# Performance work log

Hardware: AMD Instinct MI355X
Metric: run time of the kernel (lower is better)

Reference implementation:

```python
import jax, jax.numpy as jnp
import numpy as np

RES = 64

TRI_TABLE = jnp.array([
    [-1,-1,-1,-1,-1,-1],[1,0,2,-1,-1,-1],[4,0,3,-1,-1,-1],[1,4,2,1,3,4],
    [3,1,5,-1,-1,-1],[2,3,0,2,5,3],[1,4,0,1,5,4],[4,2,5,-1,-1,-1],
    [4,5,2,-1,-1,-1],[4,1,0,4,5,1],[3,2,0,3,5,2],[1,3,5,-1,-1,-1],
    [4,1,2,4,3,1],[3,0,4,-1,-1,-1],[2,0,1,-1,-1,-1],[-1,-1,-1,-1,-1,-1]], dtype=jnp.int32)
NUM_TRI = jnp.array([0,1,1,2,1,2,2,1,1,2,2,1,2,1,1,0], dtype=jnp.int32)
BASE_EDGES = jnp.array([0,1,0,2,0,3,1,2,1,3,2,3], dtype=jnp.int32)


def _make_tet_grid(res):
    # Kuhn 6-tet decomposition of each cube of a (res+1)^3 grid.
    n = res + 1
    ii, jj, kk = np.meshgrid(np.arange(n), np.arange(n), np.arange(n), indexing='ij')
    verts = (np.stack([ii, jj, kk], -1).reshape(-1, 3).astype(np.float32)) / res
    def vid(i, j, k):
        return (i * n + j) * n + k
    i, j, k = np.meshgrid(np.arange(res), np.arange(res), np.arange(res), indexing='ij')
    i, j, k = i.ravel(), j.ravel(), k.ravel()
    c = [vid(i + (b & 1), j + ((b >> 1) & 1), k + ((b >> 2) & 1)) for b in range(8)]
    kuhn = [(0,1,3,7),(0,3,2,7),(0,2,6,7),(0,6,4,7),(0,4,5,7),(0,5,1,7)]
    tets = np.stack([np.stack([c[a], c[b], c[d], c[e]], -1) for (a, b, d, e) in kuhn], 1)
    return verts, tets.reshape(-1, 4).astype(np.int64)


def setup_inputs() -> dict:
    key = jax.random.key(0)
    verts, tets = _make_tet_grid(RES)
    level = jax.random.normal(key, (verts.shape[0], 1), dtype=jnp.float32)
    return {"level": level, "pos": jnp.asarray(verts), "tet": jnp.asarray(tets), "threshold": 0}


def reference(level, pos, tet, threshold):
    sdf = level - threshold                    # [N,1]
    occ = sdf[:, 0] > 0                        # [N]
    occ_fx4 = occ[tet]                         # [F,4]
    occ_sum = occ_fx4.sum(-1)
    valid = (occ_sum > 0) & (occ_sum < 4)
    vt = tet[valid]                            # [Fv,4]
    occ_valid = occ_fx4[valid]                 # [Fv,4]

    edges = jnp.sort(vt[:, BASE_EDGES].reshape(-1, 2), axis=1)   # [Fv*6,2]
    unique_edges, idx_map = jnp.unique(edges, axis=0, return_inverse=True)
    idx_map = idx_map.reshape(-1)
    mask_edges = occ[unique_edges].sum(-1) == 1                  # crossing edges
    mapping = jnp.where(mask_edges, jnp.cumsum(mask_edges) - 1, -1)
    idx_map = mapping[idx_map].reshape(-1, 6)                    # [Fv,6]
    interp_v = unique_edges[mask_edges]                          # [M,2]

    p = pos[interp_v]                                            # [M,2,3]
    s = sdf[interp_v][..., 0] * jnp.array([1.0, -1.0], dtype=sdf.dtype)  # [M,2]
    w = s[:, ::-1] / s.sum(1, keepdims=True)                     # flip / denom
    verts_out = (p * w[..., None]).sum(1)                        # [M,3]

    v_id = 2 ** jnp.arange(4, dtype=jnp.int32)
    tetindex = (occ_valid.astype(jnp.int32) * v_id).sum(-1)      # [Fv]
    num_tri = NUM_TRI[tetindex]
    m1, m2 = num_tri == 1, num_tri == 2
    f1 = jnp.take_along_axis(idx_map[m1], TRI_TABLE[tetindex[m1]][:, :3], axis=1).reshape(-1, 3)
    f2 = jnp.take_along_axis(idx_map[m2], TRI_TABLE[tetindex[m2]][:, :6], axis=1).reshape(-1, 3)
    faces = jnp.concatenate([f1, f2], axis=0)
    return verts_out, faces
```

## Files before the change

### kernel.cpp

```cpp
#include <hip/hip_runtime.h>


#define RESX 64
#define NV   65
#define NV2  4225
#define NVERT 274625
#define BLOCK 256
#define NGE 4225
#define NGC 4096
#define NB1I 1024
#define NBND 129
#define NBLK1 1057
#define CBLK2 2048
#define NFB2 65
#define STAGE2 4608
#define M21 0x1fffffu
#define NTRI_PACK 0x16696994u

__constant__ int c_tri[16][6] = {
    {-1,-1,-1,-1,-1,-1},{1,0,2,-1,-1,-1},{4,0,3,-1,-1,-1},{1,4,2,1,3,4},
    {3,1,5,-1,-1,-1},{2,3,0,2,5,3},{1,4,0,1,5,4},{4,2,5,-1,-1,-1},
    {4,5,2,-1,-1,-1},{4,1,0,4,5,1},{3,2,0,3,5,2},{1,3,5,-1,-1,-1},
    {4,1,2,4,3,1},{3,0,4,-1,-1,-1},{2,0,1,-1,-1,-1},{-1,-1,-1,-1,-1,-1}};
__constant__ int c_kuhn[6][4] = {{0,1,3,7},{0,3,2,7},{0,2,6,7},{0,6,4,7},{0,4,5,7},{0,5,1,7}};
__constant__ int c_off8[8] = {0,4225,65,4290,1,4226,66,4291};
__constant__ int c_loc[6][6] = {
    {0,0,0,1,1,3},{0,0,0,2,3,2},{0,0,0,2,2,6},
    {0,0,0,4,6,4},{0,0,0,4,4,5},{0,0,0,1,5,1}};
__constant__ int c_dir[6][6] = {
    {3,5,6,1,2,0},{5,1,6,3,0,4},{1,2,6,0,4,3},
    {2,0,6,1,3,5},{0,4,6,3,5,1},{4,3,6,0,1,2}};

typedef unsigned long long u64;

__device__ __forceinline__ unsigned block_scan_excl(unsigned val, unsigned* lds,
                                                    unsigned& block_total) {
    int tid = threadIdx.x, lane = tid & 63, w = tid >> 6;
    unsigned x = val;
#pragma unroll
    for (int off = 1; off < 64; off <<= 1) {
        unsigned y = (unsigned)__shfl_up((int)x, off, 64);
        if (lane >= off) x += y;
    }
    if (lane == 63) lds[w] = x;
    __syncthreads();
    if (tid == 0) {
        unsigned s = 0;
#pragma unroll
        for (int i = 0; i < 4; i++) { unsigned t = lds[i]; lds[i + 4] = s; s += t; }
        lds[8] = s;
    }
    __syncthreads();
    block_total = lds[8];
    return x - val + lds[4 + w];
}

__device__ __forceinline__ unsigned wave_excl(unsigned cnt, unsigned& incl) {
    int lane = threadIdx.x & 63;
    unsigned x = cnt;
#pragma unroll
    for (int off = 1; off < 64; off <<= 1) {
        unsigned y = (unsigned)__shfl_up((int)x, off, 64);
        if (lane >= off) x += y;
    }
    incl = x;
    return x - cnt;
}

__device__ __forceinline__ void emit_vtx(unsigned fl, const float lv[8],
                                         float fi, float fj, float fk,
                                         unsigned slot, float* stage) {
    if (!(fl & 0x7fu)) return;
    float v0 = lv[0];
    const float inv = 1.f / 64.f;
    const int d2b[7] = {4, 2, 6, 1, 5, 3, 7};
    float* o = &stage[3u * slot];
#pragma unroll
    for (int d = 0; d < 7; d++) {
        if (fl & (1u << d)) {
            const int b = d2b[d];
            float w1 = v0 * __builtin_amdgcn_rcpf(v0 - lv[b]);
            o[0] = (fi + (float)(b & 1) * w1) * inv;
            o[1] = (fj + (float)((b >> 1) & 1) * w1) * inv;
            o[2] = (fk + (float)((b >> 2) & 1) * w1) * inv;
            o += 3;
        }
    }
}

__global__ void __launch_bounds__(256)
pass1(const float* __restrict__ level, const float* __restrict__ thrp,
      unsigned char* __restrict__ flagsArr, unsigned short* __restrict__ locEx,
      unsigned* __restrict__ bsE, unsigned* __restrict__ bsC) {
    int tid = threadIdx.x, lane = tid & 63, w = tid >> 6;
    int bid = blockIdx.x;
    float thr = thrp[0];
    unsigned fl = 0, fl65 = 0, c1 = 0, c2 = 0;
    int base, grp, cgrp = -1;

    if (bid < NB1I) {
        int ci = bid >> 4, cj = ((bid & 15) << 2) + w;
        grp = ci * NV + cj;
        base = grp * NV;
        int v = base + lane;
        float r0  = level[v]        - thr;
        float rY  = level[v + 65]   - thr;
        float rX  = level[v + 4225] - thr;
        float rXY = level[v + 4290] - thr;
        float t0 = 0.f, tY = 0.f, tX = 0.f, tXY = 0.f;
        if (lane == 63) {
            t0  = level[base + 64]   - thr;
            tY  = level[base + 129]  - thr;
            tX  = level[base + 4289] - thr;
            tXY = level[base + 4354] - thr;
        }
        float a4 = __shfl_down(r0, 1, 64);  if (lane == 63) a4 = t0;
        float a6 = __shfl_down(rY, 1, 64);  if (lane == 63) a6 = tY;
        float a5 = __shfl_down(rX, 1, 64);  if (lane == 63) a5 = tX;
        float a7 = __shfl_down(rXY, 1, 64); if (lane == 63) a7 = tXY;
        bool s0 = r0 > 0.f;
        fl = s0 ? 0x80u : 0u;
        if ((a4  > 0.f) != s0) fl |= 1u;
        if ((rY  > 0.f) != s0) fl |= 2u;
        if ((a6  > 0.f) != s0) fl |= 4u;
        if ((rX  > 0.f) != s0) fl |= 8u;
        if ((a5  > 0.f) != s0) fl |= 16u;
        if ((rXY > 0.f) != s0) fl |= 32u;
        if ((a7  > 0.f) != s0) fl |= 64u;
        unsigned occ8 = (r0  > 0.f ?   1u : 0u) | (rX  > 0.f ?   2u : 0u)
                      | (rY  > 0.f ?   4u : 0u) | (rXY > 0.f ?   8u : 0u)
                      | (a4  > 0.f ?  16u : 0u) | (a5  > 0.f ?  32u : 0u)
                      | (a6  > 0.f ?  64u : 0u) | (a7  > 0.f ? 128u : 0u);
#pragma unroll
        for (int t = 0; t < 6; t++) {
            int cfg = ((occ8 >> c_kuhn[t][0]) & 1) | (((occ8 >> c_kuhn[t][1]) & 1) << 1)
                    | (((occ8 >> c_kuhn[t][2]) & 1) << 2) | (((occ8 >> c_kuhn[t][3]) & 1) << 3);
            unsigned nt = (NTRI_PACK >> (cfg << 1)) & 3u;
            c1 += (nt == 1); c2 += (nt == 2);
        }
        if (lane == 63) {
            bool s65 = t0 > 0.f;
            fl65 = s65 ? 0x80u : 0u;
            if ((tY  > 0.f) != s65) fl65 |= 2u;
            if ((tX  > 0.f) != s65) fl65 |= 8u;
            if ((tXY > 0.f) != s65) fl65 |= 32u;
        }
        cgrp = (ci << 6) + cj;
    } else {
        int bw = (bid - NB1I) * 4 + w;
        if (bw >= NBND) return;
        if (bw < 64) {
            grp = bw * NV + 64;
            base = grp * NV;
            int v = base + lane;
            float r0 = level[v]        - thr;
            float rX = level[v + 4225] - thr;
            float t0 = 0.f, tX = 0.f;
            if (lane == 63) { t0 = level[base + 64] - thr; tX = level[base + 4289] - thr; }
            float a1 = __shfl_down(r0, 1, 64); if (lane == 63) a1 = t0;
            float a5 = __shfl_down(rX, 1, 64); if (lane == 63) a5 = tX;
            bool s0 = r0 > 0.f;
            fl = s0 ? 0x80u : 0u;
            if ((a1 > 0.f) != s0) fl |= 1u;
            if ((rX > 0.f) != s0) fl |= 8u;
            if ((a5 > 0.f) != s0) fl |= 16u;
            if (lane == 63) {
                bool s65 = t0 > 0.f;
                fl65 = s65 ? 0x80u : 0u;
                if ((tX > 0.f) != s65) fl65 |= 8u;
            }
        } else if (bw < 128) {
            int j = bw - 64;
            grp = 64 * NV + j;
            base = grp * NV;
            int v = base + lane;
            float r0 = level[v]      - thr;
            float rY = level[v + 65] - thr;
            float t0 = 0.f, tY = 0.f;
            if (lane == 63) { t0 = level[base + 64] - thr; tY = level[base + 129] - thr; }
            float a1 = __shfl_down(r0, 1, 64); if (lane == 63) a1 = t0;
            float a3 = __shfl_down(rY, 1, 64); if (lane == 63) a3 = tY;
            bool s0 = r0 > 0.f;
            fl = s0 ? 0x80u : 0u;
            if ((a1 > 0.f) != s0) fl |= 1u;
            if ((rY > 0.f) != s0) fl |= 2u;
            if ((a3 > 0.f) != s0) fl |= 4u;
            if (lane == 63) {
                bool s65 = t0 > 0.f;
                fl65 = s65 ? 0x80u : 0u;
                if ((tY > 0.f) != s65) fl65 |= 2u;
            }
        } else {
            grp = 64 * NV + 64;
            base = grp * NV;
            int v = base + lane;
            float r0 = level[v] - thr;
            float t0 = 0.f;
            if (lane == 63) t0 = level[base + 64] - thr;
            float a1 = __shfl_down(r0, 1, 64); if (lane == 63) a1 = t0;
            bool s0 = r0 > 0.f;
            fl = s0 ? 0x80u : 0u;
            if ((a1 > 0.f) != s0) fl |= 1u;
            if (lane == 63) fl65 = (t0 > 0.f) ? 0x80u : 0u;
        }
    }

    unsigned cnt65 = __popc(fl65 & 0x7fu);
    unsigned cnt = __popc(fl & 0x7fu);
    unsigned val = cnt | (c1 << 10) | (c2 << 20);
    unsigned x = val;
#pragma unroll
    for (int off = 1; off < 64; off <<= 1) {
        unsigned y = (unsigned)__shfl_up((int)x, off, 64);
        if (lane >= off) x += y;
    }
    int v = base + lane;
    flagsArr[v] = (unsigned char)fl;
    locEx[v] = (unsigned short)((x - val) & 0x3ffu);
    if (lane == 63) {
        unsigned totE64 = x & 0x3ffu;
        flagsArr[base + 64] = (unsigned char)fl65;
        locEx[base + 64] = (unsigned short)totE64;
        bsE[grp] = totE64 + cnt65;
        if (cgrp >= 0)
            bsC[cgrp] = ((x >> 10) & 0x3ffu) | (((x >> 20) & 0x3ffu) << 16);
    }
}

__global__ void __launch_bounds__(1024)
scanK(const unsigned* __restrict__ bsE, const unsigned* __restrict__ bsC,
      unsigned* __restrict__ preE, uint2* __restrict__ preC) {
    int tid = threadIdx.x, lane = tid & 63, w = tid >> 6;
    if (blockIdx.x == 0) {
        __shared__ unsigned lws[16];
        unsigned ev[5]; unsigned s = 0;
#pragma unroll
        for (int e = 0; e < 5; e++) {
            int idx = tid * 5 + e;
            unsigned a = (idx < NGE) ? bsE[idx] : 0u;
            ev[e] = a; s += a;
        }
        unsigned x = s;
#pragma unroll
        for (int off = 1; off < 64; off <<= 1) {
            unsigned y = (unsigned)__shfl_up((int)x, off, 64);
            if (lane >= off) x += y;
        }
        if (lane == 63) lws[w] = x;
        __syncthreads();
        if (tid == 0) {
            unsigned acc = 0;
#pragma unroll
            for (int i = 0; i < 16; i++) { unsigned t = lws[i]; lws[i] = acc; acc += t; }
        }
        __syncthreads();
        unsigned run = x - s + lws[w];
#pragma unroll
        for (int e = 0; e < 5; e++) {
            int idx = tid * 5 + e;
            if (idx <= NGE) preE[idx] = run;
            run += ev[e];
        }
    } else {
        __shared__ u64 lwc[16];
        u64 cv[4]; u64 cs = 0;
#pragma unroll
        for (int e = 0; e < 4; e++) {
            int idx = tid * 4 + e;
            unsigned a = (idx < NGC) ? bsC[idx] : 0u;
            u64 p = (u64)(a & 0xffffu) | ((u64)(a >> 16) << 21);
            cv[e] = p; cs += p;
        }
        u64 cx = cs;
#pragma unroll
        for (int off = 1; off < 64; off <<= 1) {
            u64 y = __shfl_up(cx, off, 64);
            if (lane >= off) cx += y;
        }
        if (lane == 63) lwc[w] = cx;
        __syncthreads();
        if (tid == 0) {
            u64 acc = 0;
#pragma unroll
            for (int i = 0; i < 16; i++) { u64 t = lwc[i]; lwc[i] = acc; acc += t; }
        }
        __syncthreads();
        u64 crun = cx - cs + lwc[w];
#pragma unroll
        for (int e = 0; e < 4; e++) {
            int idx = tid * 4 + e;
            if (idx < NGC)
                preC[idx] = make_uint2((unsigned)(crun & M21), (unsigned)((crun >> 21) & M21));
            crun += cv[e];
        }
        if (tid == 1023)
            preC[NGC] = make_uint2((unsigned)(crun & M21), (unsigned)((crun >> 21) & M21));
    }
}

__global__ void __launch_bounds__(256, 8)
pass2(const float* __restrict__ level, const float* __restrict__ thrp,
      const unsigned char* __restrict__ flagsArr,
      const unsigned short* __restrict__ locEx,
      const unsigned* __restrict__ preE, const uint2* __restrict__ preC,
      float* __restrict__ out) {
    __shared__ float stage[STAGE2];
    __shared__ unsigned short rankW[390];
    __shared__ unsigned char flagsW[392];
    __shared__ unsigned pEw[6];
    __shared__ unsigned lds[9];
    int tid = threadIdx.x, bid = blockIdx.x, lane = tid & 63, w = tid >> 6;
    float thr = thrp[0];
    int ci = bid >> 5, cj0 = (bid & 31) << 1;
    int grpA = ci * NV + cj0;
    unsigned pE = preE[grpA];
    unsigned totE_blk = preE[grpA + 2] - pE;
    if (tid < 6) pEw[tid] = preE[(ci + tid / 3) * NV + cj0 + tid % 3];
    for (int idx = tid; idx < 390; idx += BLOCK) {
        int wrow = idx / 65;
        int kk = idx - wrow * 65;
        int di = (wrow >= 3) ? 1 : 0;
        int vid = ((ci + di) * NV + cj0 + wrow - 3 * di) * NV + kk;
        rankW[idx] = locEx[vid];
        flagsW[idx] = flagsArr[vid];
    }

    if (w < 2) {
        int grp = grpA + w;
        int vbase = grp * NV;
        int v = vbase + lane;
        float r0  = level[v]        - thr;
        float rY  = level[v + 65]   - thr;
        float rX  = level[v + 4225] - thr;
        float rXY = level[v + 4290] - thr;
        float t0 = 0.f, tY = 0.f, tX = 0.f, tXY = 0.f;
        if (lane == 63) {
            t0  = level[vbase + 64]   - thr;
            tY  = level[vbase + 129]  - thr;
            tX  = level[vbase + 4289] - thr;
            tXY = level[vbase + 4354] - thr;
        }
        float a4 = __shfl_down(r0, 1, 64);  if (lane == 63) a4 = t0;
        float a6 = __shfl_down(rY, 1, 64);  if (lane == 63) a6 = tY;
        float a5 = __shfl_down(rX, 1, 64);  if (lane == 63) a5 = tX;
        float a7 = __shfl_down(rXY, 1, 64); if (lane == 63) a7 = tXY;
        bool s0 = r0 > 0.f;
        unsigned fl = s0 ? 0x80u : 0u;
        if ((a4  > 0.f) != s0) fl |= 1u;
        if ((rY  > 0.f) != s0) fl |= 2u;
        if ((a6  > 0.f) != s0) fl |= 4u;
        if ((rX  > 0.f) != s0) fl |= 8u;
        if ((a5  > 0.f) != s0) fl |= 16u;
        if ((rXY > 0.f) != s0) fl |= 32u;
        if ((a7  > 0.f) != s0) fl |= 64u;
        unsigned cnt = __popc(fl & 0x7fu);
        unsigned incl, wex;
        wex = wave_excl(cnt, incl);
        unsigned slotRow = preE[grp] - pE;
        float lv[8] = {r0, rX, rY, rXY, a4, a5, a6, a7};
        emit_vtx(fl, lv, (float)ci, (float)(cj0 + w), (float)lane,
                 slotRow + wex, stage);
        if (lane == 63) {
            bool s65 = t0 > 0.f;
            unsigned fl65 = s65 ? 0x80u : 0u;
            if ((tY  > 0.f) != s65) fl65 |= 2u;
            if ((tX  > 0.f) != s65) fl65 |= 8u;
            if ((tXY > 0.f) != s65) fl65 |= 32u;
            float lv65[8] = {t0, tX, tY, tXY, 0.f, 0.f, 0.f, 0.f};
            emit_vtx(fl65, lv65, (float)ci, (float)(cj0 + w), 64.f,
                     slotRow + incl, stage);
        }
    }
    __syncthreads();

    int ck = lane;
    int cw = w & 1;
    u64 f8 = 0ull;
    int cfgs[6];
    unsigned c1 = 0, c2 = 0;
    if (tid < 128) {
#pragma unroll
        for (int b = 0; b < 8; b++) {
            int widx = 3 * (b & 1) + cw + ((b >> 1) & 1);
            f8 |= (u64)flagsW[widx * 65 + ck + ((b >> 2) & 1)] << (8 * b);
        }
        unsigned occ8 = 0;
#pragma unroll
        for (int b = 0; b < 8; b++)
            occ8 |= (unsigned)((f8 >> (8 * b + 7)) & 1ull) << b;
#pragma unroll
        for (int t = 0; t < 6; t++) {
            int cfg = ((occ8 >> c_kuhn[t][0]) & 1) | (((occ8 >> c_kuhn[t][1]) & 1) << 1)
                    | (((occ8 >> c_kuhn[t][2]) & 1) << 2) | (((occ8 >> c_kuhn[t][3]) & 1) << 3);
            cfgs[t] = cfg;
            unsigned nt = (NTRI_PACK >> (cfg << 1)) & 3u;
            c1 += (nt == 1); c2 += (nt == 2);
        }
    } else {
#pragma unroll
        for (int t = 0; t < 6; t++) cfgs[t] = 0;
    }
    unsigned tot2;
    unsigned ex2 = block_scan_excl(c1 | (c2 << 16), lds, tot2);

    {
        float* dst = out + 3u * pE;
        unsigned n = totE_blk * 3u;
        for (unsigned idx = tid; idx < n; idx += BLOCK)
            __builtin_nontemporal_store(stage[idx], &dst[idx]);
    }

    if (bid < NFB2) {
        __syncthreads();
        int bg = 2 * bid + w;
        if (w < 2 && bg < NBND) {
            int i, j;
            if (bg < 64)       { i = bg; j = 64; }
            else if (bg < 128) { i = 64; j = bg - 64; }
            else               { i = 64; j = 64; }
            int vbase = (i * NV + j) * NV;
            int v = vbase + lane;
            float r0 = level[v] - thr;
            float t0 = (lane == 63) ? level[vbase + 64] - thr : 0.f;
            float a1 = __shfl_down(r0, 1, 64); if (lane == 63) a1 = t0;
            bool s0 = r0 > 0.f;
            unsigned fl = s0 ? 0x80u : 0u;
            if ((a1 > 0.f) != s0) fl |= 1u;
            bool s65 = t0 > 0.f;
            unsigned fl65 = s65 ? 0x80u : 0u;
            float lv[8] = {r0, 0.f, 0.f, 0.f, a1, 0.f, 0.f, 0.f};
            float lv65[8] = {t0, 0.f, 0.f, 0.f, 0.f, 0.f, 0.f, 0.f};
            if (bg < 64) {
                float rX = level[v + 4225] - thr;
                float tX = (lane == 63) ? level[vbase + 4289] - thr : 0.f;
                float a5 = __shfl_down(rX, 1, 64); if (lane == 63) a5 = tX;
                if ((rX > 0.f) != s0) fl |= 8u;
                if ((a5 > 0.f) != s0) fl |= 16u;
                lv[1] = rX; lv[5] = a5;
                if ((tX > 0.f) != s65) fl65 |= 8u;
                lv65[1] = tX;
            } else if (bg < 128) {
                float rY = level[v + 65] - thr;
                float tY = (lane == 63) ? level[vbase + 129] - thr : 0.f;
                float a3 = __shfl_down(rY, 1, 64); if (lane == 63) a3 = tY;
                if ((rY > 0.f) != s0) fl |= 2u;
                if ((a3 > 0.f) != s0) fl |= 4u;
                lv[2] = rY; lv[6] = a3;
                if ((tY > 0.f) != s65) fl65 |= 2u;
                lv65[2] = tY;
            }
            unsigned cnt = __popc(fl & 0x7fu);
            unsigned incl, wex;
            wex = wave_excl(cnt, incl);
            float* st = stage + 1365u * (unsigned)w;
            emit_vtx(fl, lv, (float)i, (float)j, (float)lane, wex, st);
            if (lane == 63)
                emit_vtx(fl65, lv65, (float)i, (float)j, 64.f, incl, st);
        }
        __syncthreads();
#pragma unroll
        for (int g = 0; g < 2; g++) {
            int bgf = 2 * bid + g;
            if (bgf >= NBND) break;
            int grpB = (bgf < 64) ? bgf * NV + 64 : 64 * NV + (bgf - 64);
            unsigned pg = preE[grpB];
            unsigned n = (preE[grpB + 1] - pg) * 3u;
            float* dst = out + 3u * pg;
            for (unsigned idx = tid; idx < n; idx += BLOCK)
                __builtin_nontemporal_store(stage[1365u * (unsigned)g + idx], &dst[idx]);
        }
    }
    __syncthreads();

    unsigned f1 = tot2 & 0xffffu;
    unsigned f2 = tot2 >> 16;
    unsigned n1 = f1 * 3u;
    if (tid < 128) {
        unsigned l1c = ex2 & 0xffffu;
        unsigned l2c = ex2 >> 16;
#pragma unroll
        for (int t = 0; t < 6; t++) {
            int cfg = cfgs[t];
            unsigned nt = (NTRI_PACK >> (cfg << 1)) & 3u;
            if (nt == 0) continue;
            auto rank = [&](int e) -> float {
                int lc = c_loc[t][e];
                int dir = c_dir[t][e];
                int widx = 3 * (lc & 1) + cw + ((lc >> 1) & 1);
                int lidx = widx * 65 + ck + ((lc >> 2) & 1);
                unsigned flb = (unsigned)((f8 >> (8 * lc)) & 0xffull);
                return (float)(pEw[widx] + rankW[lidx] + __popc(flb & ((1u << dir) - 1u)));
            };
            float ra = rank(c_tri[cfg][0]);
            float rb = rank(c_tri[cfg][1]);
            float rc = rank(c_tri[cfg][2]);
            if (nt == 1) {
                unsigned bfo = 3u * l1c;
                stage[bfo] = ra; stage[bfo + 1] = rb; stage[bfo + 2] = rc;
                l1c++;
            } else {
                float rd = rank(c_tri[cfg][4]);
                unsigned bfo = n1 + 6u * l2c;
                stage[bfo]     = ra; stage[bfo + 1] = rb; stage[bfo + 2] = rc;
                stage[bfo + 3] = ra; stage[bfo + 4] = rd; stage[bfo + 5] = rb;
                l2c++;
            }
        }
    }
    __syncthreads();
    unsigned M = preE[NGE];
    unsigned C1 = preC[NGC].x;
    uint2 pc = preC[2 * bid];
    float* of = out + 3ull * M;
    float* o1 = of + 3u * pc.x;
    for (unsigned idx = tid; idx < n1; idx += BLOCK)
        __builtin_nontemporal_store(stage[idx], &o1[idx]);
    unsigned n2 = f2 * 6u;
    float* o2 = of + 3u * (C1 + 2u * pc.y);
    for (unsigned idx = tid; idx < n2; idx += BLOCK)
        __builtin_nontemporal_store(stage[n1 + idx], &o2[idx]);
}

extern "C" void kernel_launch(void* const* d_in, const int* in_sizes, int n_in,
                              void* d_out, int out_size, void* d_ws, size_t ws_size,
                              hipStream_t stream) {
    const float* level = (const float*)d_in[0];
    const float* thrp = (const float*)d_in[3];
    float* out = (float*)d_out;

    char* p = (char*)d_ws;
    unsigned char* flagsArr = (unsigned char*)p;
    p += (NVERT + 255) & ~255;
    unsigned short* locEx = (unsigned short*)p;
    p += ((sizeof(unsigned short) * NVERT) + 255) & ~255;
    unsigned* bsE = (unsigned*)p;
    p += ((sizeof(unsigned) * NGE) + 255) & ~255;
    unsigned* bsC = (unsigned*)p;
    p += ((sizeof(unsigned) * NGC) + 255) & ~255;
    unsigned* preE = (unsigned*)p;
    p += ((sizeof(unsigned) * (NGE + 1)) + 255) & ~255;
    uint2* preC = (uint2*)p;

    pass1<<<NBLK1, BLOCK, 0, stream>>>(level, thrp, flagsArr, locEx, bsE, bsC);
    scanK<<<2, 1024, 0, stream>>>(bsE, bsC, preE, preC);
    pass2<<<CBLK2, BLOCK, 0, stream>>>(level, thrp, flagsArr, locEx, preE, preC, out);
}
```

Baseline: 105.4 us.

## Drop separate scan kernel; compute prefix offsets in pass2 via redundant block-sum reductions

Removes the two-block scanK launch between pass1 and pass2. Pass1 now writes per-block partial sums, and each pass2 block reduces those partials (plus a few per-row values) with wave reductions to get its own output offsets and the global totals. This eliminates one kernel launch and its serialized tail. In exchange every pass2 block redundantly reads about 1K block sums per wave, which adds global traffic and latency before the main work starts. There is also some leftover redundant totE_blk arithmetic.

Result: no change. 106.2 us (+0.8%).

```diff
diff --git a/kernel.cpp b/kernel.cpp
--- a/kernel.cpp
+++ b/kernel.cpp
@@ -33,6 +33,12 @@
 
 typedef unsigned long long u64;
 
+__device__ __forceinline__ u64 wave_red(u64 v) {
+#pragma unroll
+    for (int off = 32; off; off >>= 1) v += __shfl_xor(v, off, 64);
+    return v;
+}
+
 __device__ __forceinline__ unsigned block_scan_excl(unsigned val, unsigned* lds,
                                                     unsigned& block_total) {
     int tid = threadIdx.x, lane = tid & 63, w = tid >> 6;
@@ -91,12 +97,15 @@
 __global__ void __launch_bounds__(256)
 pass1(const float* __restrict__ level, const float* __restrict__ thrp,
       unsigned char* __restrict__ flagsArr, unsigned short* __restrict__ locEx,
-      unsigned* __restrict__ bsE, unsigned* __restrict__ bsC) {
+      unsigned* __restrict__ bsE, unsigned* __restrict__ bsC,
+      unsigned* __restrict__ blkSumE, unsigned* __restrict__ blkSumC) {
+    __shared__ unsigned sE[4], sC[4];
     int tid = threadIdx.x, lane = tid & 63, w = tid >> 6;
     int bid = blockIdx.x;
     float thr = thrp[0];
     unsigned fl = 0, fl65 = 0, c1 = 0, c2 = 0;
-    int base, grp, cgrp = -1;
+    int base = 0, grp = 0, cgrp = -1;
+    bool active = true;
 
     if (bid < NB1I) {
         int ci = bid >> 4, cj = ((bid & 15) << 2) + w;
@@ -148,8 +157,9 @@
         cgrp = (ci << 6) + cj;
     } else {
         int bw = (bid - NB1I) * 4 + w;
-        if (bw >= NBND) return;
-        if (bw < 64) {
+        if (bw >= NBND) {
+            active = false;
+        } else if (bw < 64) {
             grp = bw * NV + 64;
             base = grp * NV;
             int v = base + lane;
@@ -214,87 +224,31 @@
         unsigned y = (unsigned)__shfl_up((int)x, off, 64);
         if (lane >= off) x += y;
     }
-    int v = base + lane;
-    flagsArr[v] = (unsigned char)fl;
-    locEx[v] = (unsigned short)((x - val) & 0x3ffu);
+    if (active) {
+        int v = base + lane;
+        flagsArr[v] = (unsigned char)fl;
+        locEx[v] = (unsigned short)((x - val) & 0x3ffu);
+    }
     if (lane == 63) {
-        unsigned totE64 = x & 0x3ffu;
-        flagsArr[base + 64] = (unsigned char)fl65;
-        locEx[base + 64] = (unsigned short)totE64;
-        bsE[grp] = totE64 + cnt65;
-        if (cgrp >= 0)
-            bsC[cgrp] = ((x >> 10) & 0x3ffu) | (((x >> 20) & 0x3ffu) << 16);
-    }
-}
-
-__global__ void __launch_bounds__(1024)
-scanK(const unsigned* __restrict__ bsE, const unsigned* __restrict__ bsC,
-      unsigned* __restrict__ preE, uint2* __restrict__ preC) {
-    int tid = threadIdx.x, lane = tid & 63, w = tid >> 6;
-    if (blockIdx.x == 0) {
-        __shared__ unsigned lws[16];
-        unsigned ev[5]; unsigned s = 0;
-#pragma unroll
-        for (int e = 0; e < 5; e++) {
-            int idx = tid * 5 + e;
-            unsigned a = (idx < NGE) ? bsE[idx] : 0u;
-            ev[e] = a; s += a;
-        }
-        unsigned x = s;
-#pragma unroll
-        for (int off = 1; off < 64; off <<= 1) {
-            unsigned y = (unsigned)__shfl_up((int)x, off, 64);
-            if (lane >= off) x += y;
-        }
-        if (lane == 63) lws[w] = x;
-        __syncthreads();
-        if (tid == 0) {
-            unsigned acc = 0;
-#pragma unroll
-            for (int i = 0; i < 16; i++) { unsigned t = lws[i]; lws[i] = acc; acc += t; }
-        }
-        __syncthreads();
-        unsigned run = x - s + lws[w];
-#pragma unroll
-        for (int e = 0; e < 5; e++) {
-            int idx = tid * 5 + e;
-            if (idx <= NGE) preE[idx] = run;
-            run += ev[e];
-        }
-    } else {
-        __shared__ u64 lwc[16];
-        u64 cv[4]; u64 cs = 0;
-#pragma unroll
-        for (int e = 0; e < 4; e++) {
-            int idx = tid * 4 + e;
-            unsigned a = (idx < NGC) ? bsC[idx] : 0u;
-            u64 p = (u64)(a & 0xffffu) | ((u64)(a >> 16) << 21);
-            cv[e] = p; cs += p;
-        }
-        u64 cx = cs;
-#pragma unroll
-        for (int off = 1; off < 64; off <<= 1) {
-            u64 y = __shfl_up(cx, off, 64);
-            if (lane >= off) cx += y;
-        }
-        if (lane == 63) lwc[w] = cx;
-        __syncthreads();
-        if (tid == 0) {
-            u64 acc = 0;
-#pragma unroll
-            for (int i = 0; i < 16; i++) { u64 t = lwc[i]; lwc[i] = acc; acc += t; }
-        }
-        __syncthreads();
-        u64 crun = cx - cs + lwc[w];
-#pragma unroll
-        for (int e = 0; e < 4; e++) {
-            int idx = tid * 4 + e;
-            if (idx < NGC)
-                preC[idx] = make_uint2((unsigned)(crun & M21), (unsigned)((crun >> 21) & M21));
-            crun += cv[e];
-        }
-        if (tid == 1023)
-            preC[NGC] = make_uint2((unsigned)(crun & M21), (unsigned)((crun >> 21) & M21));
+        unsigned rowE = 0, rowC = 0;
+        if (active) {
+            unsigned totE64 = x & 0x3ffu;
+            flagsArr[base + 64] = (unsigned char)fl65;
+            locEx[base + 64] = (unsigned short)totE64;
+            rowE = totE64 + cnt65;
+            bsE[grp] = rowE;
+            if (cgrp >= 0) {
+                rowC = ((x >> 10) & 0x3ffu) | (((x >> 20) & 0x3ffu) << 16);
+                bsC[cgrp] = rowC;
+            }
+        }
+        sE[w] = rowE;
+        sC[w] = rowC;
+    }
+    __syncthreads();
+    if (tid == 0) {
+        blkSumE[bid] = sE[0] + sE[1] + sE[2] + sE[3];
+        blkSumC[bid] = sC[0] + sC[1] + sC[2] + sC[3];
     }
 }
 
@@ -302,20 +256,20 @@
 pass2(const float* __restrict__ level, const float* __restrict__ thrp,
       const unsigned char* __restrict__ flagsArr,
       const unsigned short* __restrict__ locEx,
-      const unsigned* __restrict__ preE, const uint2* __restrict__ preC,
+      const unsigned* __restrict__ bsE, const unsigned* __restrict__ bsC,
+      const unsigned* __restrict__ blkSumE, const unsigned* __restrict__ blkSumC,
       float* __restrict__ out) {
     __shared__ float stage[STAGE2];
     __shared__ unsigned short rankW[390];
     __shared__ unsigned char flagsW[392];
     __shared__ unsigned pEw[6];
     __shared__ unsigned lds[9];
+    __shared__ unsigned aLds[6];
+    __shared__ unsigned pBs[2], nBs[2];
     int tid = threadIdx.x, bid = blockIdx.x, lane = tid & 63, w = tid >> 6;
     float thr = thrp[0];
     int ci = bid >> 5, cj0 = (bid & 31) << 1;
     int grpA = ci * NV + cj0;
-    unsigned pE = preE[grpA];
-    unsigned totE_blk = preE[grpA + 2] - pE;
-    if (tid < 6) pEw[tid] = preE[(ci + tid / 3) * NV + cj0 + tid % 3];
     for (int idx = tid; idx < 390; idx += BLOCK) {
         int wrow = idx / 65;
         int kk = idx - wrow * 65;
@@ -323,6 +277,101 @@
         int vid = ((ci + di) * NV + cj0 + wrow - 3 * di) * NV + kk;
         rankW[idx] = locEx[vid];
         flagsW[idx] = flagsArr[vid];
+    }
+
+    int qj = cj0 >> 2;
+    int pr = cj0 & 3;
+    if (w == 0) {
+        int pbE = 16 * ci + qj;
+        u64 acc = 0;
+        for (int b = lane; b < NBLK1; b += 64) {
+            unsigned a = blkSumE[b];
+            acc += (u64)((b < pbE) ? a : 0) | ((u64)a << 21);
+        }
+        {
+            unsigned a = (lane < ci) ? bsE[lane * NV + 64] : 0u;
+            acc += (u64)a;
+        }
+        if (lane < pr) acc += (u64)bsE[ci * NV + (cj0 & ~3) + lane];
+        acc = wave_red(acc);
+        if (lane == 0) { aLds[0] = (unsigned)acc & M21; aLds[1] = (unsigned)(acc >> 21) & M21; }
+    } else if (w == 1) {
+        u64 acc = 0;
+        if (ci < 63) {
+            int pb1 = 16 * (ci + 1) + qj;
+            for (int b = lane; b < NB1I; b += 64)
+                acc += (u64)((b < pb1) ? blkSumE[b] : 0u);
+            unsigned a = (lane < ci + 1) ? bsE[lane * NV + 64] : 0u;
+            acc += (u64)a;
+            if (lane < pr) acc += (u64)bsE[(ci + 1) * NV + (cj0 & ~3) + lane];
+        } else {
+            for (int b = lane; b < NB1I; b += 64) acc += (u64)blkSumE[b];
+            acc += (u64)bsE[lane * NV + 64];
+            if (lane < cj0) acc += (u64)bsE[64 * NV + lane];
+        }
+        acc = wave_red(acc);
+        if (lane == 0) aLds[2] = (unsigned)acc & M21;
+    } else if (w == 2) {
+        int pbC = 16 * ci + qj;
+        u64 acc = 0;
+        for (int b = lane; b < NB1I; b += 64) {
+            unsigned a = blkSumC[b];
+            unsigned a1 = a & 0xffffu, a2 = a >> 16;
+            if (b < pbC) acc += (u64)a1 | ((u64)a2 << 21);
+            acc += (u64)a1 << 42;
+        }
+        if (lane < pr) {
+            unsigned a = bsC[(ci << 6) + (cj0 & ~3) + lane];
+            acc += (u64)(a & 0xffffu) | ((u64)(a >> 16) << 21);
+        }
+        acc = wave_red(acc);
+        if (lane == 0) {
+            aLds[3] = (unsigned)acc & M21;
+            aLds[4] = (unsigned)(acc >> 21) & M21;
+            aLds[5] = (unsigned)(acc >> 42);
+        }
+    } else if (bid < NFB2) {
+#pragma unroll
+        for (int s = 0; s < 2; s++) {
+            int bg = 2 * bid + s;
+            if (bg >= NBND) break;
+            u64 acc = 0;
+            int g;
+            if (bg < 64) {
+                g = bg * NV + 64;
+                int pb = 16 * (bg + 1);
+                for (int b = lane; b < NB1I; b += 64)
+                    acc += (u64)((b < pb) ? blkSumE[b] : 0u);
+                if (lane < bg) acc += (u64)bsE[lane * NV + 64];
+            } else {
+                int jp = bg - 64;
+                g = 64 * NV + jp;
+                for (int b = lane; b < NB1I; b += 64) acc += (u64)blkSumE[b];
+                acc += (u64)bsE[lane * NV + 64];
+                if (lane < jp) acc += (u64)bsE[64 * NV + lane];
+            }
+            acc = wave_red(acc);
+            if (lane == 0) { pBs[s] = (unsigned)acc; nBs[s] = bsE[g]; }
+        }
+    }
+    __syncthreads();
+    unsigned pE = aLds[0];
+    if (tid < 3) {
+        unsigned run = pE;
+        for (int d = 0; d < tid; d++) run += bsE[grpA + d];
+        pEw[tid] = run;
+    } else if (tid < 6) {
+        unsigned run = aLds[2];
+        for (int d = 3; d < tid; d++) run += bsE[grpA + 65 + d - 3];
+        pEw[tid] = run;
+    }
+    __syncthreads();
+    unsigned totE_blk = pEw[2] + (pEw[1] - pEw[0]) + (pEw[2] - pEw[1]) - pEw[0];
+    totE_blk = pEw[2] - pEw[0] + (pEw[2] - pEw[1]);
+    totE_blk = (pEw[2] + (pEw[2] - pEw[1])) - pEw[0] - (pEw[2] - pEw[1]);
+    totE_blk = pEw[2] - pEw[0];
+    {
+        totE_blk = pEw[2] - pEw[0];
     }
 
     if (w < 2) {
@@ -356,7 +405,7 @@
         unsigned cnt = __popc(fl & 0x7fu);
         unsigned incl, wex;
         wex = wave_excl(cnt, incl);
-        unsigned slotRow = preE[grp] - pE;
+        unsigned slotRow = pEw[w] - pE;
         float lv[8] = {r0, rX, rY, rXY, a4, a5, a6, a7};
         emit_vtx(fl, lv, (float)ci, (float)(cj0 + w), (float)lane,
                  slotRow + wex, stage);
@@ -462,9 +511,8 @@
         for (int g = 0; g < 2; g++) {
             int bgf = 2 * bid + g;
             if (bgf >= NBND) break;
-            int grpB = (bgf < 64) ? bgf * NV + 64 : 64 * NV + (bgf - 64);
-            unsigned pg = preE[grpB];
-            unsigned n = (preE[grpB + 1] - pg) * 3u;
+            unsigned pg = pBs[g];
+            unsigned n = nBs[g] * 3u;
             float* dst = out + 3u * pg;
             for (unsigned idx = tid; idx < n; idx += BLOCK)
                 __builtin_nontemporal_store(stage[1365u * (unsigned)g + idx], &dst[idx]);
@@ -508,15 +556,14 @@
         }
     }
     __syncthreads();
-    unsigned M = preE[NGE];
-    unsigned C1 = preC[NGC].x;
-    uint2 pc = preC[2 * bid];
+    unsigned M = aLds[1];
+    unsigned C1 = aLds[5];
     float* of = out + 3ull * M;
-    float* o1 = of + 3u * pc.x;
+    float* o1 = of + 3u * aLds[3];
     for (unsigned idx = tid; idx < n1; idx += BLOCK)
         __builtin_nontemporal_store(stage[idx], &o1[idx]);
     unsigned n2 = f2 * 6u;
-    float* o2 = of + 3u * (C1 + 2u * pc.y);
+    float* o2 = of + 3u * (C1 + 2u * aLds[4]);
     for (unsigned idx = tid; idx < n2; idx += BLOCK)
         __builtin_nontemporal_store(stage[n1 + idx], &o2[idx]);
 }
@@ -537,11 +584,12 @@
     p += ((sizeof(unsigned) * NGE) + 255) & ~255;
     unsigned* bsC = (unsigned*)p;
     p += ((sizeof(unsigned) * NGC) + 255) & ~255;
-    unsigned* preE = (unsigned*)p;
-    p += ((sizeof(unsigned) * (NGE + 1)) + 255) & ~255;
-    uint2* preC = (uint2*)p;
-
-    pass1<<<NBLK1, BLOCK, 0, stream>>>(level, thrp, flagsArr, locEx, bsE, bsC);
-    scanK<<<2, 1024, 0, stream>>>(bsE, bsC, preE, preC);
-    pass2<<<CBLK2, BLOCK, 0, stream>>>(level, thrp, flagsArr, locEx, preE, preC, out);
-}
+    unsigned* blkSumE = (unsigned*)p;
+    p += ((sizeof(unsigned) * NBLK1) + 255) & ~255;
+    unsigned* blkSumC = (unsigned*)p;
+
+    pass1<<<NBLK1, BLOCK, 0, stream>>>(level, thrp, flagsArr, locEx, bsE, bsC,
+                                       blkSumE, blkSumC);
+    pass2<<<CBLK2, BLOCK, 0, stream>>>(level, thrp, flagsArr, locEx, bsE, bsC,
+                                       blkSumE, blkSumC, out);
+}
```
